# Kernel tuning notes

Hardware: AMD Instinct MI355X
Metric: run time of the kernel (lower is better)

Reference implementation:

```python
import jax, jax.numpy as jnp
import numpy as np
from jax import lax

N = 1_000_000   # nodes
E = 16_000_000  # edges
K1, K2, K3 = 100_000, 10_000, 2_500  # ceil(ratio*n) per pooling stage
EPS = 1e-5


def cgconv(x, src, dst, edge_attr, edge_valid, Wf, bf, Ws, bs, gamma, beta, num_nodes):
    # z_ij = [x_i, x_j, e_ij]  (PyG: i = target = dst, j = source = src)
    z = jnp.concatenate([x[dst], x[src], edge_attr], axis=-1)          # [E,3]
    m = jax.nn.sigmoid(z @ Wf + bf) * jax.nn.softplus(z @ Ws + bs)     # [E,1]
    m = m * edge_valid[:, None].astype(m.dtype)
    aggr = jax.ops.segment_sum(m, dst, num_segments=num_nodes)         # [n,1]
    # BatchNorm1d (training-mode batch stats, biased var), then residual
    mean = aggr.mean(axis=0)
    var = aggr.var(axis=0)
    bn = gamma * (aggr - mean) / jnp.sqrt(var + EPS) + beta
    return bn + x


def topk_pool(x, src, dst, edge_attr, edge_valid, w, k, num_nodes):
    # Original torch code broadcasts x[N,1]*w[C] -> sum(-1) == x*sum(w); tanh nonlinearity.
    score = jnp.tanh(x[:, 0] * jnp.sum(w) / jnp.linalg.norm(w))        # [n]
    top_scores, perm = lax.top_k(score, k)
    x_new = x[perm] * top_scores[:, None]
    mask = jnp.zeros((num_nodes,), bool).at[perm].set(True)
    new_idx = jnp.zeros((num_nodes,), jnp.int32).at[perm].set(jnp.arange(k, dtype=jnp.int32))
    ev = edge_valid & mask[src] & mask[dst]
    return x_new, new_idx[src], new_idx[dst], edge_attr, ev


def setup_inputs() -> dict:
    key = jax.random.key(0)
    ks = jax.random.split(key, 24)
    d = {}
    d["x"] = jax.random.normal(ks[0], (N, 1), jnp.float32)
    d["edge_attr"] = jax.random.uniform(ks[1], (E, 1), jnp.float32)
    d["src"] = jax.random.randint(ks[2], (E,), 0, N, jnp.int32)
    d["dst"] = jax.random.randint(ks[3], (E,), 0, N, jnp.int32)
    d["batch"] = jnp.zeros((N,), jnp.int32)
    p = lambda k, shp: jax.random.normal(k, shp, jnp.float32) * 0.1
    d["Wf1"], d["bf1"] = p(ks[4], (3, 1)), p(ks[5], (1,))
    d["Ws1"], d["bs1"] = p(ks[6], (3, 1)), p(ks[7], (1,))
    d["g1"], d["be1"] = jnp.ones((1,), jnp.float32), jnp.zeros((1,), jnp.float32)
    d["Wf2"], d["bf2"] = p(ks[8], (3, 1)), p(ks[9], (1,))
    d["Ws2"], d["bs2"] = p(ks[10], (3, 1)), p(ks[11], (1,))
    d["g2"], d["be2"] = jnp.ones((1,), jnp.float32), jnp.zeros((1,), jnp.float32)
    d["pw1"] = p(ks[12], (800,))
    d["pw2"] = p(ks[13], (80,))
    d["pw3"] = p(ks[14], (8,))
    d["Wl1"], d["bl1"] = p(ks[15], (1, 8)), p(ks[16], (8,))
    d["Wl2"], d["bl2"] = p(ks[17], (8, 2)), p(ks[18], (2,))
    return d


def reference(x, edge_attr, Wf1, bf1, Ws1, bs1, g1, be1, Wf2, bf2, Ws2, bs2, g2, be2,
              pw1, pw2, pw3, Wl1, bl1, Wl2, bl2, src, dst, batch):
    ev = jnp.ones((E,), bool)
    x = cgconv(x, src, dst, edge_attr, ev, Wf1, bf1, Ws1, bs1, g1, be1, N)
    x, s, dd, ea, ev = topk_pool(x, src, dst, edge_attr, ev, pw1, K1, N)
    x = cgconv(x, s, dd, ea, ev, Wf2, bf2, Ws2, bs2, g2, be2, K1)
    x, s, dd, ea, ev = topk_pool(x, s, dd, ea, ev, pw2, K2, K1)
    x, s, dd, ea, ev = topk_pool(x, s, dd, ea, ev, pw3, K3, K2)
    h = jax.nn.relu(x @ Wl1 + bl1)
    # dropout is identity in eval/reference mode
    return jax.nn.log_softmax(h @ Wl2 + bl2, axis=1)
```

## Files before the change

### kernel.cpp

```cpp
#include <hip/hip_runtime.h>
#include <math.h>

#define CHUNK 4096
#define NB2   256
#define BSH   12
#define CAP   24
#define CAPW  49
#define FG    16
#define RND   1024
#define EPB   16384

typedef int      i32x4 __attribute__((ext_vector_type(4)));
typedef float    f32x4 __attribute__((ext_vector_type(4)));
typedef unsigned u32x2 __attribute__((ext_vector_type(2)));

__device__ __forceinline__ i32x4 ntld4i(const int* p)   { return __builtin_nontemporal_load((const i32x4*)p); }
__device__ __forceinline__ f32x4 ntld4f(const float* p) { return __builtin_nontemporal_load((const f32x4*)p); }

__device__ __forceinline__ float sigmoidf_(float x) {
    if (x >= 0.0f) { float e = expf(-x); return 1.0f / (1.0f + e); }
    float e = expf(x); return e / (1.0f + e);
}
__device__ __forceinline__ float softplusf_(float x) {
    return fmaxf(x, 0.0f) + log1pf(expf(-fabsf(x)));
}
__device__ __forceinline__ unsigned key_desc(float f) {
    unsigned u = __float_as_uint(f);
    unsigned ka = (u & 0x80000000u) ? ~u : (u | 0x80000000u);
    return ~ka;
}
__device__ __forceinline__ float edge_m(float xd, float xs, float a,
                                        float wf0, float wf1, float wf2, float b0,
                                        float ws0, float ws1, float ws2, float b1) {
    float f = xd * wf0 + xs * wf1 + a * wf2 + b0;
    float g = xd * ws0 + xs * ws1 + a * ws2 + b1;
    return sigmoidf_(f) * softplusf_(g);
}

__global__ void k_consts(const float* __restrict__ pw1, const float* __restrict__ pw2,
                         const float* __restrict__ pw3, float* __restrict__ consts,
                         int n1, int n2, int n3) {
    const float* w; int n;
    if (blockIdx.x == 0)      { w = pw1; n = n1; }
    else if (blockIdx.x == 1) { w = pw2; n = n2; }
    else                      { w = pw3; n = n3; }
    __shared__ float s1[256], s2[256];
    float a = 0.f, b = 0.f;
    for (int i = threadIdx.x; i < n; i += 256) { float v = w[i]; a += v; b += v * v; }
    s1[threadIdx.x] = a; s2[threadIdx.x] = b; __syncthreads();
    for (int o = 128; o > 0; o >>= 1) {
        if (threadIdx.x < o) { s1[threadIdx.x] += s1[threadIdx.x + o]; s2[threadIdx.x] += s2[threadIdx.x + o]; }
        __syncthreads();
    }
    if (threadIdx.x == 0) consts[blockIdx.x] = s1[0] / sqrtf(s2[0]);
}

__global__ void __launch_bounds__(256) k_ehist2(const int* __restrict__ dst,
                                                unsigned* __restrict__ hist,
                                                int e0, int e1) {
    __shared__ unsigned h[NB2];
    int t = threadIdx.x;
    h[t] = 0;
    __syncthreads();
    int cs = e0 + blockIdx.x * EPB;
    int ce = cs + EPB; if (ce > e1) ce = e1;
    for (int eb = cs; eb < ce; eb += RND) {
        int i = eb + t * 4;
        if (eb + RND <= ce) {
            i32x4 d4 = ntld4i(dst + i);
            atomicAdd(&h[((unsigned)d4.x) >> BSH], 1u);
            atomicAdd(&h[((unsigned)d4.y) >> BSH], 1u);
            atomicAdd(&h[((unsigned)d4.z) >> BSH], 1u);
            atomicAdd(&h[((unsigned)d4.w) >> BSH], 1u);
        } else {
            #pragma unroll
            for (int j = 0; j < 4; ++j)
                if (i + j < ce) atomicAdd(&h[((unsigned)dst[i + j]) >> BSH], 1u);
        }
    }
    __syncthreads();
    hist[(size_t)blockIdx.x * NB2 + t] = h[t];
}

__global__ void k_scanA(const unsigned* __restrict__ hist, unsigned* __restrict__ offs,
                        unsigned* __restrict__ tot, int G) {
    int d = blockIdx.x, ND = gridDim.x, t = threadIdx.x;
    __shared__ unsigned s[256];
    unsigned carry = 0;
    for (int tile = 0; tile * 256 < G; ++tile) {
        int g = tile * 256 + t;
        unsigned v = (g < G) ? hist[(size_t)g * ND + d] : 0u;
        s[t] = v; __syncthreads();
        for (int o = 1; o < 256; o <<= 1) {
            unsigned u = (t >= o) ? s[t - o] : 0u;
            __syncthreads();
            s[t] += u; __syncthreads();
        }
        if (g < G) offs[(size_t)g * ND + d] = s[t] - v + carry;
        unsigned tl = s[255]; __syncthreads();
        carry += tl;
    }
    if (t == 0) tot[d] = carry;
}

__global__ void k_scanB(const unsigned* __restrict__ tot, unsigned* __restrict__ base,
                        int ND, unsigned rmask) {
    __shared__ unsigned s[256];
    int t = threadIdx.x;
    unsigned carry = 0;
    for (int tile = 0; tile * 256 < ND; ++tile) {
        int d = tile * 256 + t;
        unsigned v = (d < ND) ? ((tot[d] + rmask) & ~rmask) : 0u;
        s[t] = v; __syncthreads();
        for (int o = 1; o < 256; o <<= 1) {
            unsigned u = (t >= o) ? s[t - o] : 0u;
            __syncthreads();
            s[t] += u; __syncthreads();
        }
        if (d < ND) base[d] = s[t] - v + carry;
        unsigned tl = s[255]; __syncthreads();
        carry += tl;
    }
    if (t == 0) base[ND] = carry;
}

__global__ void __launch_bounds__(256) k_part(
        const float* __restrict__ x, const float* __restrict__ ea,
        const int* __restrict__ src, const int* __restrict__ dst,
        const float* __restrict__ Wf, const float* __restrict__ bf,
        const float* __restrict__ Ws, const float* __restrict__ bs,
        const unsigned* __restrict__ offs, const unsigned* __restrict__ binBase,
        uint2* __restrict__ rec, int e0, int e1) {
    __shared__ unsigned stage[NB2 * CAPW];
    __shared__ unsigned gcur[NB2], fil[NB2];
    int t = threadIdx.x;
    gcur[t] = binBase[t] + offs[(size_t)blockIdx.x * NB2 + t];
    fil[t] = 0;
    __syncthreads();
    int cs = e0 + blockIdx.x * EPB;
    int ce = cs + EPB; if (ce > e1) ce = e1;
    float wf0 = Wf[0], wf1 = Wf[1], wf2 = Wf[2], b0 = bf[0];
    float ws0 = Ws[0], ws1 = Ws[1], ws2 = Ws[2], b1 = bs[0];
    for (int rb = cs; rb < ce; rb += RND) {
        int s4[4], d4[4]; float a4[4]; bool vl[4];
        int eb = rb + t * 4;
        if (rb + RND <= ce) {
            i32x4 sv = ntld4i(src + eb);
            i32x4 dv = ntld4i(dst + eb);
            f32x4 av = ntld4f(ea + eb);
            s4[0]=sv.x; s4[1]=sv.y; s4[2]=sv.z; s4[3]=sv.w;
            d4[0]=dv.x; d4[1]=dv.y; d4[2]=dv.z; d4[3]=dv.w;
            a4[0]=av.x; a4[1]=av.y; a4[2]=av.z; a4[3]=av.w;
            vl[0]=vl[1]=vl[2]=vl[3]=true;
        } else {
            #pragma unroll
            for (int j = 0; j < 4; ++j) {
                int e = eb + j;
                vl[j] = e < ce;
                s4[j] = vl[j] ? src[e] : 0;
                d4[j] = vl[j] ? dst[e] : 0;
                a4[j] = vl[j] ? ea[e]  : 0.f;
            }
        }
        #pragma unroll
        for (int j = 0; j < 4; ++j) {
            if (!vl[j]) continue;
            int d = d4[j];
            float m = edge_m(x[d], x[s4[j]], a4[j], wf0, wf1, wf2, b0, ws0, ws1, ws2, b1);
            unsigned bin = ((unsigned)d) >> BSH;
            unsigned dl  = (unsigned)(d & ((1 << BSH) - 1));
            unsigned slot = atomicAdd(&fil[bin], 1u);
            if (slot < CAP) {
                stage[bin * CAPW + 2 * slot]     = __float_as_uint(m);
                stage[bin * CAPW + 2 * slot + 1] = dl;
            } else {
                rec[gcur[bin] + slot] = make_uint2(__float_as_uint(m), dl);
            }
        }
        __syncthreads();
        {
            unsigned c = fil[t], g = gcur[t];
            unsigned* st = &stage[t * CAPW];
            if (c > CAP) {
                for (unsigned k = 0; k < CAP; ++k)
                    rec[g + k] = make_uint2(st[2 * k], st[2 * k + 1]);
                gcur[t] = g + c; fil[t] = 0;
            } else {
                unsigned ngrp = c >> 4;
                if (ngrp) {
                    unsigned nfl = ngrp << 4;
                    for (unsigned k = 0; k < nfl; ++k)
                        rec[g + k] = make_uint2(st[2 * k], st[2 * k + 1]);
                    unsigned rem = c - nfl;
                    for (unsigned k = 0; k < rem; ++k) {
                        st[2 * k]     = st[2 * (nfl + k)];
                        st[2 * k + 1] = st[2 * (nfl + k) + 1];
                    }
                    gcur[t] = g + nfl; fil[t] = rem;
                }
            }
        }
        __syncthreads();
    }
    {
        unsigned c = fil[t], g = gcur[t];
        unsigned* st = &stage[t * CAPW];
        unsigned cc = c < CAP ? c : CAP;
        for (unsigned k = 0; k < cc; ++k)
            rec[g + k] = make_uint2(st[2 * k], st[2 * k + 1]);
    }
}

__global__ void __launch_bounds__(256) k_aggr2(
        const uint2* __restrict__ rec, const unsigned* __restrict__ base,
        const unsigned* __restrict__ tot, float* __restrict__ aggr,
        float* __restrict__ stats, int N, int accumulate, int doStats) {
    __shared__ float acc[1 << BSH];
    int t = threadIdx.x, b = blockIdx.x;
    for (int i = t; i < (1 << BSH); i += 256) acc[i] = 0.f;
    __syncthreads();
    unsigned lo = base[b], hi = lo + tot[b];
    for (unsigned i = lo + t; i < hi; i += 256) {
        u32x2 r = __builtin_nontemporal_load((const u32x2*)&rec[i]);
        atomicAdd(&acc[r.y], __uint_as_float(r.x));
    }
    __syncthreads();
    int nb = b << BSH;
    float s = 0.f, q = 0.f;
    for (int i = t; i < (1 << BSH); i += 256) {
        int node = nb + i;
        if (node < N) {
            float v = acc[i];
            if (accumulate) v += aggr[node];
            aggr[node] = v;
            if (doStats) { s += v; q += v * v; }
        }
    }
    if (doStats) {
        __shared__ float s1[256], s2[256];
        s1[t] = s; s2[t] = q; __syncthreads();
        for (int o = 128; o > 0; o >>= 1) {
            if (t < o) { s1[t] += s1[t + o]; s2[t] += s2[t + o]; }
            __syncthreads();
        }
        if (t == 0) { atomicAdd(&stats[0], s1[0]); atomicAdd(&stats[1], s2[0]); }
    }
}

__global__ void k_conv1(const float* __restrict__ x, const float* __restrict__ ea,
                        const int* __restrict__ src, const int* __restrict__ dst,
                        const float* __restrict__ Wf, const float* __restrict__ bf,
                        const float* __restrict__ Ws, const float* __restrict__ bs,
                        float* __restrict__ aggr, int E) {
    int e = blockIdx.x * blockDim.x + threadIdx.x;
    if (e >= E) return;
    int s = src[e], d = dst[e];
    atomicAdd(&aggr[d], edge_m(x[d], x[s], ea[e], Wf[0], Wf[1], Wf[2], bf[0],
                               Ws[0], Ws[1], Ws[2], bs[0]));
}

__global__ void __launch_bounds__(256) k_conv2(
        const float* __restrict__ x2, const float* __restrict__ ea,
        const int* __restrict__ src, const int* __restrict__ dst,
        const int* __restrict__ nidx,
        const float* __restrict__ Wf, const float* __restrict__ bf,
        const float* __restrict__ Ws, const float* __restrict__ bs,
        float* __restrict__ aggr, int E) {
    int base = (blockIdx.x * 256 + threadIdx.x) * 4;
    if (base >= E) return;
    float wf0 = Wf[0], wf1 = Wf[1], wf2 = Wf[2], b0 = bf[0];
    float ws0 = Ws[0], ws1 = Ws[1], ws2 = Ws[2], b1 = bs[0];
    int d4[4]; int cnt;
    if (base + 4 <= E) {
        i32x4 dv = ntld4i(dst + base);
        d4[0]=dv.x; d4[1]=dv.y; d4[2]=dv.z; d4[3]=dv.w;
        cnt = 4;
    } else {
        cnt = E - base;
        for (int j = 0; j < cnt; ++j) d4[j] = dst[base + j];
    }
    #pragma unroll
    for (int j = 0; j < 4; ++j) {
        if (j >= cnt) break;
        int nd = nidx[d4[j]];
        if (nd < 0) continue;
        int sv = __builtin_nontemporal_load(src + base + j);
        int ns = nidx[sv];
        if (ns < 0) continue;
        float a = __builtin_nontemporal_load(ea + base + j);
        atomicAdd(&aggr[nd], edge_m(x2[nd], x2[ns], a, wf0, wf1, wf2, b0, ws0, ws1, ws2, b1));
    }
}

__global__ void k_stats(const float* __restrict__ a, int n, float* __restrict__ stats) {
    float s = 0.f, q = 0.f;
    int stride = gridDim.x * blockDim.x;
    for (int i = blockIdx.x * blockDim.x + threadIdx.x; i < n; i += stride) {
        float v = a[i]; s += v; q += v * v;
    }
    __shared__ float s1[256], s2[256];
    s1[threadIdx.x] = s; s2[threadIdx.x] = q; __syncthreads();
    for (int o = 128; o > 0; o >>= 1) {
        if (threadIdx.x < o) { s1[threadIdx.x] += s1[threadIdx.x + o]; s2[threadIdx.x] += s2[threadIdx.x + o]; }
        __syncthreads();
    }
    if (threadIdx.x == 0) { atomicAdd(&stats[0], s1[0]); atomicAdd(&stats[1], s2[0]); }
}

__global__ void k_bn(const float* __restrict__ aggr, const float* __restrict__ xin,
                     const float* __restrict__ stats, const float* __restrict__ g,
                     const float* __restrict__ be, float* __restrict__ xout,
                     int n, float invn, const float* __restrict__ consts, int ci,
                     unsigned* __restrict__ keys, unsigned* __restrict__ vals) {
    int i = blockIdx.x * blockDim.x + threadIdx.x;
    if (i >= n) return;
    float mean = stats[0] * invn;
    float var  = stats[1] * invn - mean * mean;
    float inv  = 1.0f / sqrtf(var + 1e-5f);
    float v = g[0] * (aggr[i] - mean) * inv + be[0] + xin[i];
    xout[i] = v;
    if (keys) {
        float s = tanhf(v * consts[ci]);
        keys[i] = key_desc(s);
        vals[i] = (unsigned)i;
    }
}

__global__ void k_hist(const unsigned* __restrict__ keys, unsigned* __restrict__ hist,
                       int n, int shift) {
    __shared__ unsigned h[256];
    int t = threadIdx.x;
    h[t] = 0;
    __syncthreads();
    int base = blockIdx.x * CHUNK;
    if (base + CHUNK <= n) {
        #pragma unroll
        for (int it = 0; it < CHUNK / 1024; ++it) {
            int i = base + it * 1024 + t * 4;
            const unsigned* p = keys + i;
            unsigned k0 = p[0], k1 = p[1], k2 = p[2], k3 = p[3];
            atomicAdd(&h[(k0 >> shift) & 255u], 1u);
            atomicAdd(&h[(k1 >> shift) & 255u], 1u);
            atomicAdd(&h[(k2 >> shift) & 255u], 1u);
            atomicAdd(&h[(k3 >> shift) & 255u], 1u);
        }
    } else {
        int end = n;
        for (int i = base + t; i < end; i += 256)
            atomicAdd(&h[(keys[i] >> shift) & 255u], 1u);
    }
    __syncthreads();
    hist[blockIdx.x * 256 + t] = h[t];
}

__global__ void __launch_bounds__(256) k_scatter(const unsigned* __restrict__ keys,
                                                 const unsigned* __restrict__ vals,
                                                 unsigned* __restrict__ okeys,
                                                 unsigned* __restrict__ ovals,
                                                 const unsigned* __restrict__ offs,
                                                 const unsigned* __restrict__ base_,
                                                 int n, int shift) {
    __shared__ unsigned run[256];
    __shared__ unsigned offl[256];
    __shared__ unsigned wcnt[4][256];
    __shared__ unsigned wpre[4][256];
    int t = threadIdx.x;
    int wave = t >> 6, lane = t & 63;
    run[t] = 0;
    offl[t] = offs[(size_t)blockIdx.x * 256 + t] + base_[t];
    __syncthreads();
    int cbase = blockIdx.x * CHUNK;
    const int GROUPS = CHUNK / 256;
    for (int gix = 0; gix < GROUPS; ++gix) {
        int i = cbase + gix * 256 + t;
        bool active = i < n;
        unsigned k = active ? keys[i] : 0u;
        unsigned v = active ? vals[i] : 0u;
        unsigned d = (k >> shift) & 255u;
        unsigned long long amask = __ballot(active);
        unsigned long long bb[8];
        #pragma unroll
        for (int bit = 0; bit < 8; ++bit) bb[bit] = __ballot(active && ((d >> bit) & 1u));
        unsigned long long m = amask;
        #pragma unroll
        for (int bit = 0; bit < 8; ++bit) m &= ((d >> bit) & 1u) ? bb[bit] : ~bb[bit];
        unsigned rk = (unsigned)__popcll(m & ((1ull << lane) - 1ull));
        #pragma unroll
        for (int j = 0; j < 4; ++j) {
            unsigned dd = (unsigned)lane + j * 64u;
            unsigned long long mm = amask;
            #pragma unroll
            for (int bit = 0; bit < 8; ++bit) mm &= ((dd >> bit) & 1u) ? bb[bit] : ~bb[bit];
            wcnt[wave][dd] = (unsigned)__popcll(mm);
        }
        __syncthreads();
        {
            unsigned r = run[t];
            unsigned c0 = wcnt[0][t], c1 = wcnt[1][t], c2 = wcnt[2][t], c3 = wcnt[3][t];
            wpre[0][t] = r;
            wpre[1][t] = r + c0;
            wpre[2][t] = r + c0 + c1;
            wpre[3][t] = r + c0 + c1 + c2;
            run[t] = r + c0 + c1 + c2 + c3;
        }
        __syncthreads();
        if (active) {
            unsigned pos = offl[d] + wpre[wave][d] + rk;
            okeys[pos] = k;
            ovals[pos] = v;
        }
    }
}

__global__ void k_pool(const unsigned* __restrict__ perm, const float* __restrict__ xin,
                       const float* __restrict__ consts, int ci,
                       float* __restrict__ xout, int* __restrict__ newidx, int k,
                       unsigned* __restrict__ okeys, unsigned* __restrict__ ovals, int nci) {
    int r = blockIdx.x * blockDim.x + threadIdx.x;
    if (r >= k) return;
    unsigned p = perm[r];
    float xv = xin[p];
    float s = tanhf(xv * consts[ci]);
    float o = xv * s;
    xout[r] = o;
    if (newidx) newidx[p] = r;
    if (okeys) {
        float s2 = tanhf(o * consts[nci]);
        okeys[r] = key_desc(s2);
        ovals[r] = (unsigned)r;
    }
}

__global__ void __launch_bounds__(1024) k_smallsort(
        unsigned* __restrict__ kIn, unsigned* __restrict__ vIn,
        unsigned* __restrict__ kTmp, unsigned* __restrict__ vTmp,
        int n, int k3, const float* __restrict__ xin,
        const float* __restrict__ consts, int ci,
        const float* __restrict__ Wl1, const float* __restrict__ bl1,
        const float* __restrict__ Wl2, const float* __restrict__ bl2,
        float* __restrict__ out) {
    __shared__ unsigned hist[256], sc[256], run[256], offl[256];
    __shared__ unsigned wcnt[16][256];
    __shared__ unsigned wpre[16][256];
    int t = threadIdx.x;
    int wave = t >> 6, lane = t & 63;
    unsigned *ki = kIn, *vi = vIn, *ko = kTmp, *vo = vTmp;
    for (int p = 0; p < 4; ++p) {
        int shift = p * 8;
        if (t < 256) hist[t] = 0;
        __syncthreads();
        for (int i = t; i < n; i += 1024)
            atomicAdd(&hist[(ki[i] >> shift) & 255u], 1u);
        __syncthreads();
        if (t < 256) sc[t] = hist[t];
        __syncthreads();
        for (int o = 1; o < 256; o <<= 1) {
            unsigned u = 0;
            if (t < 256 && t >= o) u = sc[t - o];
            __syncthreads();
            if (t < 256) sc[t] += u;
            __syncthreads();
        }
        if (t < 256) { offl[t] = sc[t] - hist[t]; run[t] = 0; }
        __syncthreads();
        int G = (n + 1023) / 1024;
        for (int gix = 0; gix < G; ++gix) {
            int i = gix * 1024 + t;
            bool active = i < n;
            unsigned k = active ? ki[i] : 0u;
            unsigned v = active ? vi[i] : 0u;
            unsigned d = (k >> shift) & 255u;
            unsigned long long amask = __ballot(active);
            unsigned long long bb[8];
            #pragma unroll
            for (int bit = 0; bit < 8; ++bit) bb[bit] = __ballot(active && ((d >> bit) & 1u));
            unsigned long long m = amask;
            #pragma unroll
            for (int bit = 0; bit < 8; ++bit) m &= ((d >> bit) & 1u) ? bb[bit] : ~bb[bit];
            unsigned rk = (unsigned)__popcll(m & ((1ull << lane) - 1ull));
            #pragma unroll
            for (int j = 0; j < 4; ++j) {
                unsigned dd = (unsigned)lane + j * 64u;
                unsigned long long mm = amask;
                #pragma unroll
                for (int bit = 0; bit < 8; ++bit) mm &= ((dd >> bit) & 1u) ? bb[bit] : ~bb[bit];
                wcnt[wave][dd] = (unsigned)__popcll(mm);
            }
            __syncthreads();
            if (t < 256) {
                unsigned acc = run[t];
                #pragma unroll
                for (int w2 = 0; w2 < 16; ++w2) { wpre[w2][t] = acc; acc += wcnt[w2][t]; }
                run[t] = acc;
            }
            __syncthreads();
            if (active) {
                unsigned pos = offl[d] + wpre[wave][d] + rk;
                ko[pos] = k;
                vo[pos] = v;
            }
            __syncthreads();
        }
        unsigned* tp;
        tp = ki; ki = ko; ko = tp;
        tp = vi; vi = vo; vo = tp;
        __syncthreads();
    }
    float c = consts[ci];
    float b20 = bl2[0], b21 = bl2[1];
    for (int r = t; r < k3; r += 1024) {
        unsigned pidx = vIn[r];
        float xv = xin[pidx];
        float s = tanhf(xv * c);
        float o = xv * s;
        float l0 = b20, l1 = b21;
        #pragma unroll
        for (int j = 0; j < 8; ++j) {
            float h = fmaxf(o * Wl1[j] + bl1[j], 0.0f);
            l0 += h * Wl2[2 * j];
            l1 += h * Wl2[2 * j + 1];
        }
        float mx = fmaxf(l0, l1);
        float lse = mx + logf(expf(l0 - mx) + expf(l1 - mx));
        out[2 * r]     = l0 - lse;
        out[2 * r + 1] = l1 - lse;
    }
}

static void sort_pairs(hipStream_t stream, unsigned* kA, unsigned* vA,
                       unsigned* kB, unsigned* vB, unsigned* hist, unsigned* offs,
                       unsigned* tot, unsigned* base, int n) {
    int G = (n + CHUNK - 1) / CHUNK;
    unsigned *ki = kA, *vi = vA, *ko = kB, *vo = vB;
    for (int p = 0; p < 4; ++p) {
        int shift = p * 8;
        k_hist<<<G, 256, 0, stream>>>(ki, hist, n, shift);
        k_scanA<<<256, 256, 0, stream>>>(hist, offs, tot, G);
        k_scanB<<<1, 256, 0, stream>>>(tot, base, 256, 0u);
        k_scatter<<<G, 256, 0, stream>>>(ki, vi, ko, vo, offs, base, n, shift);
        unsigned* t;
        t = ki; ki = ko; ko = t;
        t = vi; vi = vo; vo = t;
    }
}

extern "C" void kernel_launch(void* const* d_in, const int* in_sizes, int n_in,
                              void* d_out, int out_size, void* d_ws, size_t ws_size,
                              hipStream_t stream) {
    const float* x   = (const float*)d_in[0];
    const float* ea  = (const float*)d_in[1];
    const int*   src = (const int*)d_in[2];
    const int*   dst = (const int*)d_in[3];
    const float *Wf1 = (const float*)d_in[5],  *bf1 = (const float*)d_in[6];
    const float *Ws1 = (const float*)d_in[7],  *bs1 = (const float*)d_in[8];
    const float *g1  = (const float*)d_in[9],  *be1 = (const float*)d_in[10];
    const float *Wf2 = (const float*)d_in[11], *bf2 = (const float*)d_in[12];
    const float *Ws2 = (const float*)d_in[13], *bs2 = (const float*)d_in[14];
    const float *g2  = (const float*)d_in[15], *be2 = (const float*)d_in[16];
    const float *pw1 = (const float*)d_in[17], *pw2 = (const float*)d_in[18], *pw3 = (const float*)d_in[19];
    const float *Wl1 = (const float*)d_in[20], *bl1 = (const float*)d_in[21];
    const float *Wl2 = (const float*)d_in[22], *bl2 = (const float*)d_in[23];

    const int N  = in_sizes[0];
    const int E  = in_sizes[1];
    const int K1 = 100000, K2 = 10000, K3 = 2500;

    size_t off = 0;
    auto alloc = [&](size_t bytes) { size_t o = off; off = (off + bytes + 255) & ~(size_t)255; return o; };
    char* ws = (char*)d_ws;
    size_t o_x1    = alloc((size_t)N * 4);
    size_t o_nidx  = alloc((size_t)N * 4);
    size_t o_stats = alloc(256);
    size_t o_const = alloc(256);
    size_t o_tot   = alloc(4096);
    size_t o_base  = alloc(8192);
    size_t o_x2    = alloc((size_t)K1 * 4);
    size_t o_x3    = alloc((size_t)K1 * 4);
    size_t o_ag2   = alloc((size_t)K1 * 4);
    size_t o_x4    = alloc((size_t)K2 * 4);
    size_t o_x5    = alloc((size_t)K3 * 4);
    size_t o_ag1   = alloc((size_t)N * 4);
    size_t o_arena = off;

    int G1 = (N + CHUNK - 1) / CHUNK;
    size_t s_kA = 0;
    size_t s_vA = s_kA + (((size_t)N * 4 + 255) & ~(size_t)255);
    size_t s_kB = s_vA + (((size_t)N * 4 + 255) & ~(size_t)255);
    size_t s_vB = s_kB + (((size_t)N * 4 + 255) & ~(size_t)255);
    size_t s_h  = s_vB + (((size_t)N * 4 + 255) & ~(size_t)255);
    size_t s_o  = s_h  + (((size_t)G1 * 256 * 4 + 255) & ~(size_t)255);
    size_t sortSz = s_o + (size_t)G1 * 256 * 4;

    int H = 0, Eh = 0;
    size_t p_rec = 0, p_eh = 0, p_eo = 0;
    for (int h = 1; h <= 8; h <<= 1) {
        int eh_ = (E + h - 1) / h;
        eh_ = (eh_ + RND - 1) & ~(RND - 1);
        int gc_ = (eh_ + EPB - 1) / EPB;
        size_t recB = (((size_t)(eh_ + NB2 * FG) * 8) + 255) & ~(size_t)255;
        size_t ehB  = (((size_t)gc_ * NB2 * 4) + 255) & ~(size_t)255;
        size_t eoB  = (((size_t)gc_ * NB2 * 4) + 255) & ~(size_t)255;
        size_t partSz = recB + ehB + eoB;
        size_t arenaSz = partSz > sortSz ? partSz : sortSz;
        if (o_arena + arenaSz <= ws_size && N <= (NB2 << BSH)) {
            H = h; Eh = eh_;
            p_rec = 0; p_eh = p_rec + recB; p_eo = p_eh + ehB;
            break;
        }
    }

    float*    x1     = (float*)(ws + o_x1);
    int*      nidx   = (int*)(ws + o_nidx);
    float*    stats  = (float*)(ws + o_stats);
    float*    consts = (float*)(ws + o_const);
    unsigned* tot    = (unsigned*)(ws + o_tot);
    unsigned* base   = (unsigned*)(ws + o_base);
    float*    x2     = (float*)(ws + o_x2);
    float*    x3     = (float*)(ws + o_x3);
    float*    aggr2  = (float*)(ws + o_ag2);
    float*    x4     = (float*)(ws + o_x4);
    float*    aggr1  = (float*)(ws + o_ag1);
    unsigned* kA     = (unsigned*)(ws + o_arena + s_kA);
    unsigned* vA     = (unsigned*)(ws + o_arena + s_vA);
    unsigned* kB     = (unsigned*)(ws + o_arena + s_kB);
    unsigned* vB     = (unsigned*)(ws + o_arena + s_vB);
    unsigned* hist   = (unsigned*)(ws + o_arena + s_h);
    unsigned* offs   = (unsigned*)(ws + o_arena + s_o);

    hipMemsetAsync(nidx, 0xFF, (size_t)N * 4, stream);
    hipMemsetAsync(stats, 0, 64, stream);
    hipMemsetAsync(aggr2, 0, (size_t)K1 * 4, stream);

    k_consts<<<3, 256, 0, stream>>>(pw1, pw2, pw3, consts,
                                    in_sizes[17], in_sizes[18], in_sizes[19]);

    if (H > 0) {
        uint2*    rec = (uint2*)(ws + o_arena + p_rec);
        unsigned* eh  = (unsigned*)(ws + o_arena + p_eh);
        unsigned* eo  = (unsigned*)(ws + o_arena + p_eo);
        int NBN = (N + (1 << BSH) - 1) >> BSH;
        for (int h = 0; h < H; ++h) {
            int e0 = h * Eh;
            int e1 = e0 + Eh; if (e1 > E) e1 = E;
            if (e0 >= e1) break;
            int GCh = (e1 - e0 + EPB - 1) / EPB;
            k_ehist2<<<GCh, 256, 0, stream>>>(dst, eh, e0, e1);
            k_scanA<<<NB2, 256, 0, stream>>>(eh, eo, tot, GCh);
            k_scanB<<<1, 256, 0, stream>>>(tot, base, NB2, (unsigned)(FG - 1));
            k_part<<<GCh, 256, 0, stream>>>(x, ea, src, dst, Wf1, bf1, Ws1, bs1,
                                            eo, base, rec, e0, e1);
            k_aggr2<<<NBN, 256, 0, stream>>>(rec, base, tot, aggr1, stats, N,
                                             h > 0, h == H - 1 ? 1 : 0);
        }
    } else {
        hipMemsetAsync(aggr1, 0, (size_t)N * 4, stream);
        k_conv1<<<(E + 255) / 256, 256, 0, stream>>>(x, ea, src, dst, Wf1, bf1, Ws1, bs1, aggr1, E);
        k_stats<<<1024, 256, 0, stream>>>(aggr1, N, stats);
    }
    k_bn<<<(N + 255) / 256, 256, 0, stream>>>(aggr1, x, stats, g1, be1, x1, N, 1.0f / (float)N,
                                              consts, 0, kA, vA);

    sort_pairs(stream, kA, vA, kB, vB, hist, offs, tot, base, N);
    k_pool<<<(K1 + 255) / 256, 256, 0, stream>>>(vA, x1, consts, 0, x2, nidx, K1,
                                                 (unsigned*)nullptr, (unsigned*)nullptr, 0);

    k_conv2<<<(E / 4 + 255) / 256, 256, 0, stream>>>(x2, ea, src, dst, nidx,
                                                     Wf2, bf2, Ws2, bs2, aggr2, E);
    k_stats<<<256, 256, 0, stream>>>(aggr2, K1, stats + 2);
    k_bn<<<(K1 + 255) / 256, 256, 0, stream>>>(aggr2, x2, stats + 2, g2, be2, x3, K1, 1.0f / (float)K1,
                                               consts, 1, kA, vA);

    sort_pairs(stream, kA, vA, kB, vB, hist, offs, tot, base, K1);
    k_pool<<<(K2 + 255) / 256, 256, 0, stream>>>(vA, x3, consts, 1, x4, (int*)nullptr, K2,
                                                 kB, vB, 2);

    k_smallsort<<<1, 1024, 0, stream>>>(kB, vB, kA, vA, K2, K3, x4, consts, 2,
                                        Wl1, bl1, Wl2, bl2, (float*)d_out);
}
```

Baseline: 902.3 us.

## Fold bin-base scans into consumers, drop memsets, and cooperatively flush stage buffers

Removes the single-block k_scanB launches. Each consumer block (k_part, k_aggr2, k_scatter) now recomputes the 256-entry exclusive scan of totals in shared memory. The three memsets are folded into k_consts and k_bn initialization, which cuts the kernel launch count. The k_part staging flush now uses 16-lane groups per bin instead of one serial thread per bin, and k_conv2 loads src with vector loads. The trade-off is redundant per-block scans and an extra barrier sequence in each block.

```diff
diff --git a/kernel.cpp b/kernel.cpp
--- a/kernel.cpp
+++ b/kernel.cpp
@@ -39,7 +39,8 @@
 
 __global__ void k_consts(const float* __restrict__ pw1, const float* __restrict__ pw2,
                          const float* __restrict__ pw3, float* __restrict__ consts,
-                         int n1, int n2, int n3) {
+                         float* __restrict__ stats, int n1, int n2, int n3) {
+    if (blockIdx.x == 0 && threadIdx.x < 16) stats[threadIdx.x] = 0.f;
     const float* w; int n;
     if (blockIdx.x == 0)      { w = pw1; n = n1; }
     else if (blockIdx.x == 1) { w = pw2; n = n2; }
@@ -103,44 +104,33 @@
     if (t == 0) tot[d] = carry;
 }
 
-__global__ void k_scanB(const unsigned* __restrict__ tot, unsigned* __restrict__ base,
-                        int ND, unsigned rmask) {
-    __shared__ unsigned s[256];
-    int t = threadIdx.x;
-    unsigned carry = 0;
-    for (int tile = 0; tile * 256 < ND; ++tile) {
-        int d = tile * 256 + t;
-        unsigned v = (d < ND) ? ((tot[d] + rmask) & ~rmask) : 0u;
-        s[t] = v; __syncthreads();
-        for (int o = 1; o < 256; o <<= 1) {
-            unsigned u = (t >= o) ? s[t - o] : 0u;
-            __syncthreads();
-            s[t] += u; __syncthreads();
-        }
-        if (d < ND) base[d] = s[t] - v + carry;
-        unsigned tl = s[255]; __syncthreads();
-        carry += tl;
-    }
-    if (t == 0) base[ND] = carry;
-}
-
 __global__ void __launch_bounds__(256) k_part(
         const float* __restrict__ x, const float* __restrict__ ea,
         const int* __restrict__ src, const int* __restrict__ dst,
         const float* __restrict__ Wf, const float* __restrict__ bf,
         const float* __restrict__ Ws, const float* __restrict__ bs,
-        const unsigned* __restrict__ offs, const unsigned* __restrict__ binBase,
+        const unsigned* __restrict__ offs, const unsigned* __restrict__ tot,
         uint2* __restrict__ rec, int e0, int e1) {
     __shared__ unsigned stage[NB2 * CAPW];
     __shared__ unsigned gcur[NB2], fil[NB2];
     int t = threadIdx.x;
-    gcur[t] = binBase[t] + offs[(size_t)blockIdx.x * NB2 + t];
-    fil[t] = 0;
+    {
+        unsigned v = (tot[t] + FG - 1) & ~(unsigned)(FG - 1);
+        stage[t] = v; __syncthreads();
+        for (int o = 1; o < 256; o <<= 1) {
+            unsigned u = (t >= o) ? stage[t - o] : 0u;
+            __syncthreads();
+            stage[t] += u; __syncthreads();
+        }
+        gcur[t] = (stage[t] - v) + offs[(size_t)blockIdx.x * NB2 + t];
+        fil[t] = 0;
+    }
     __syncthreads();
     int cs = e0 + blockIdx.x * EPB;
     int ce = cs + EPB; if (ce > e1) ce = e1;
     float wf0 = Wf[0], wf1 = Wf[1], wf2 = Wf[2], b0 = bf[0];
     float ws0 = Ws[0], ws1 = Ws[1], ws2 = Ws[2], b1 = bs[0];
+    int sg = t >> 4, ln = t & 15;
     for (int rb = cs; rb < ce; rb += RND) {
         int s4[4], d4[4]; float a4[4]; bool vl[4];
         int eb = rb + t * 4;
@@ -178,48 +168,57 @@
             }
         }
         __syncthreads();
-        {
-            unsigned c = fil[t], g = gcur[t];
-            unsigned* st = &stage[t * CAPW];
+        for (int i = 0; i < NB2 / 16; ++i) {
+            int b = sg + (i << 4);
+            unsigned c = fil[b];
+            if (c < FG) continue;
+            unsigned g = gcur[b];
+            unsigned* st = &stage[b * CAPW];
             if (c > CAP) {
-                for (unsigned k = 0; k < CAP; ++k)
-                    rec[g + k] = make_uint2(st[2 * k], st[2 * k + 1]);
-                gcur[t] = g + c; fil[t] = 0;
+                rec[g + ln] = make_uint2(st[2 * ln], st[2 * ln + 1]);
+                if (ln < CAP - 16)
+                    rec[g + 16 + ln] = make_uint2(st[2 * (16 + ln)], st[2 * (16 + ln) + 1]);
+                if (ln == 0) { gcur[b] = g + c; fil[b] = 0; }
             } else {
-                unsigned ngrp = c >> 4;
-                if (ngrp) {
-                    unsigned nfl = ngrp << 4;
-                    for (unsigned k = 0; k < nfl; ++k)
-                        rec[g + k] = make_uint2(st[2 * k], st[2 * k + 1]);
-                    unsigned rem = c - nfl;
-                    for (unsigned k = 0; k < rem; ++k) {
-                        st[2 * k]     = st[2 * (nfl + k)];
-                        st[2 * k + 1] = st[2 * (nfl + k) + 1];
-                    }
-                    gcur[t] = g + nfl; fil[t] = rem;
-                }
+                rec[g + ln] = make_uint2(st[2 * ln], st[2 * ln + 1]);
+                unsigned rem = c - FG;
+                unsigned lo0 = 0, lo1 = 0;
+                if (ln < rem) { lo0 = st[2 * (FG + ln)]; lo1 = st[2 * (FG + ln) + 1]; }
+                if (ln < rem) { st[2 * ln] = lo0; st[2 * ln + 1] = lo1; }
+                if (ln == 0) { gcur[b] = g + FG; fil[b] = rem; }
             }
         }
         __syncthreads();
     }
+    for (int i = 0; i < NB2 / 16; ++i) {
+        int b = sg + (i << 4);
+        unsigned c = fil[b], g = gcur[b];
+        unsigned* st = &stage[b * CAPW];
+        if (ln < c) rec[g + ln] = make_uint2(st[2 * ln], st[2 * ln + 1]);
+    }
+}
+
+__global__ void __launch_bounds__(256) k_aggr2(
+        const uint2* __restrict__ rec, const unsigned* __restrict__ tot,
+        float* __restrict__ aggr, float* __restrict__ stats,
+        int N, int accumulate, int doStats) {
+    __shared__ float acc[1 << BSH];
+    __shared__ unsigned sc[256];
+    __shared__ unsigned sBase, sCnt;
+    int t = threadIdx.x, b = blockIdx.x;
     {
-        unsigned c = fil[t], g = gcur[t];
-        unsigned* st = &stage[t * CAPW];
-        unsigned cc = c < CAP ? c : CAP;
-        for (unsigned k = 0; k < cc; ++k)
-            rec[g + k] = make_uint2(st[2 * k], st[2 * k + 1]);
-    }
-}
-
-__global__ void __launch_bounds__(256) k_aggr2(
-        const uint2* __restrict__ rec, const unsigned* __restrict__ base,
-        const unsigned* __restrict__ tot, float* __restrict__ aggr,
-        float* __restrict__ stats, int N, int accumulate, int doStats) {
-    __shared__ float acc[1 << BSH];
-    int t = threadIdx.x, b = blockIdx.x;
+        unsigned v = (tot[t] + FG - 1) & ~(unsigned)(FG - 1);
+        sc[t] = v; __syncthreads();
+        for (int o = 1; o < 256; o <<= 1) {
+            unsigned u = (t >= o) ? sc[t - o] : 0u;
+            __syncthreads();
+            sc[t] += u; __syncthreads();
+        }
+        if (t == b) { sBase = sc[t] - v; sCnt = tot[t]; }
+    }
     for (int i = t; i < (1 << BSH); i += 256) acc[i] = 0.f;
     __syncthreads();
-    unsigned lo = base[b], hi = lo + tot[b];
+    unsigned lo = sBase, hi = lo + sCnt;
     for (unsigned i = lo + t; i < hi; i += 256) {
         u32x2 r = __builtin_nontemporal_load((const u32x2*)&rec[i]);
         atomicAdd(&acc[r.y], __uint_as_float(r.x));
@@ -270,22 +269,23 @@
     if (base >= E) return;
     float wf0 = Wf[0], wf1 = Wf[1], wf2 = Wf[2], b0 = bf[0];
     float ws0 = Ws[0], ws1 = Ws[1], ws2 = Ws[2], b1 = bs[0];
-    int d4[4]; int cnt;
+    int d4[4], s4[4]; int cnt;
     if (base + 4 <= E) {
         i32x4 dv = ntld4i(dst + base);
+        i32x4 sv = ntld4i(src + base);
         d4[0]=dv.x; d4[1]=dv.y; d4[2]=dv.z; d4[3]=dv.w;
+        s4[0]=sv.x; s4[1]=sv.y; s4[2]=sv.z; s4[3]=sv.w;
         cnt = 4;
     } else {
         cnt = E - base;
-        for (int j = 0; j < cnt; ++j) d4[j] = dst[base + j];
+        for (int j = 0; j < cnt; ++j) { d4[j] = dst[base + j]; s4[j] = src[base + j]; }
     }
     #pragma unroll
     for (int j = 0; j < 4; ++j) {
         if (j >= cnt) break;
         int nd = nidx[d4[j]];
         if (nd < 0) continue;
-        int sv = __builtin_nontemporal_load(src + base + j);
-        int ns = nidx[sv];
+        int ns = nidx[s4[j]];
         if (ns < 0) continue;
         float a = __builtin_nontemporal_load(ea + base + j);
         atomicAdd(&aggr[nd], edge_m(x2[nd], x2[ns], a, wf0, wf1, wf2, b0, ws0, ws1, ws2, b1));
@@ -311,19 +311,20 @@
                      const float* __restrict__ stats, const float* __restrict__ g,
                      const float* __restrict__ be, float* __restrict__ xout,
                      int n, float invn, const float* __restrict__ consts, int ci,
-                     unsigned* __restrict__ keys, unsigned* __restrict__ vals) {
+                     unsigned* __restrict__ keys, unsigned* __restrict__ vals,
+                     int* __restrict__ nidxInit, float* __restrict__ zeroArr, int nZero) {
     int i = blockIdx.x * blockDim.x + threadIdx.x;
     if (i >= n) return;
+    if (nidxInit) nidxInit[i] = -1;
+    if (zeroArr && i < nZero) zeroArr[i] = 0.f;
     float mean = stats[0] * invn;
     float var  = stats[1] * invn - mean * mean;
     float inv  = 1.0f / sqrtf(var + 1e-5f);
     float v = g[0] * (aggr[i] - mean) * inv + be[0] + xin[i];
     xout[i] = v;
-    if (keys) {
-        float s = tanhf(v * consts[ci]);
-        keys[i] = key_desc(s);
-        vals[i] = (unsigned)i;
-    }
+    float s = tanhf(v * consts[ci]);
+    keys[i] = key_desc(s);
+    vals[i] = (unsigned)i;
 }
 
 __global__ void k_hist(const unsigned* __restrict__ keys, unsigned* __restrict__ hist,
@@ -345,8 +346,7 @@
             atomicAdd(&h[(k3 >> shift) & 255u], 1u);
         }
     } else {
-        int end = n;
-        for (int i = base + t; i < end; i += 256)
+        for (int i = base + t; i < n; i += 256)
             atomicAdd(&h[(keys[i] >> shift) & 255u], 1u);
     }
     __syncthreads();
@@ -358,16 +358,26 @@
                                                  unsigned* __restrict__ okeys,
                                                  unsigned* __restrict__ ovals,
                                                  const unsigned* __restrict__ offs,
-                                                 const unsigned* __restrict__ base_,
+                                                 const unsigned* __restrict__ tot,
                                                  int n, int shift) {
     __shared__ unsigned run[256];
     __shared__ unsigned offl[256];
     __shared__ unsigned wcnt[4][256];
     __shared__ unsigned wpre[4][256];
+    __shared__ unsigned sc[256];
     int t = threadIdx.x;
     int wave = t >> 6, lane = t & 63;
-    run[t] = 0;
-    offl[t] = offs[(size_t)blockIdx.x * 256 + t] + base_[t];
+    {
+        unsigned v = tot[t];
+        sc[t] = v; __syncthreads();
+        for (int o = 1; o < 256; o <<= 1) {
+            unsigned u = (t >= o) ? sc[t - o] : 0u;
+            __syncthreads();
+            sc[t] += u; __syncthreads();
+        }
+        offl[t] = offs[(size_t)blockIdx.x * 256 + t] + (sc[t] - v);
+        run[t] = 0;
+    }
     __syncthreads();
     int cbase = blockIdx.x * CHUNK;
     const int GROUPS = CHUNK / 256;
@@ -529,15 +539,14 @@
 
 static void sort_pairs(hipStream_t stream, unsigned* kA, unsigned* vA,
                        unsigned* kB, unsigned* vB, unsigned* hist, unsigned* offs,
-                       unsigned* tot, unsigned* base, int n) {
+                       unsigned* tot, int n) {
     int G = (n + CHUNK - 1) / CHUNK;
     unsigned *ki = kA, *vi = vA, *ko = kB, *vo = vB;
     for (int p = 0; p < 4; ++p) {
         int shift = p * 8;
         k_hist<<<G, 256, 0, stream>>>(ki, hist, n, shift);
         k_scanA<<<256, 256, 0, stream>>>(hist, offs, tot, G);
-        k_scanB<<<1, 256, 0, stream>>>(tot, base, 256, 0u);
-        k_scatter<<<G, 256, 0, stream>>>(ki, vi, ko, vo, offs, base, n, shift);
+        k_scatter<<<G, 256, 0, stream>>>(ki, vi, ko, vo, offs, tot, n, shift);
         unsigned* t;
         t = ki; ki = ko; ko = t;
         t = vi; vi = vo; vo = t;
@@ -573,12 +582,10 @@
     size_t o_stats = alloc(256);
     size_t o_const = alloc(256);
     size_t o_tot   = alloc(4096);
-    size_t o_base  = alloc(8192);
     size_t o_x2    = alloc((size_t)K1 * 4);
     size_t o_x3    = alloc((size_t)K1 * 4);
     size_t o_ag2   = alloc((size_t)K1 * 4);
     size_t o_x4    = alloc((size_t)K2 * 4);
-    size_t o_x5    = alloc((size_t)K3 * 4);
     size_t o_ag1   = alloc((size_t)N * 4);
     size_t o_arena = off;
 
@@ -614,7 +621,6 @@
     float*    stats  = (float*)(ws + o_stats);
     float*    consts = (float*)(ws + o_const);
     unsigned* tot    = (unsigned*)(ws + o_tot);
-    unsigned* base   = (unsigned*)(ws + o_base);
     float*    x2     = (float*)(ws + o_x2);
     float*    x3     = (float*)(ws + o_x3);
     float*    aggr2  = (float*)(ws + o_ag2);
@@ -627,11 +633,7 @@
     unsigned* hist   = (unsigned*)(ws + o_arena + s_h);
     unsigned* offs   = (unsigned*)(ws + o_arena + s_o);
 
-    hipMemsetAsync(nidx, 0xFF, (size_t)N * 4, stream);
-    hipMemsetAsync(stats, 0, 64, stream);
-    hipMemsetAsync(aggr2, 0, (size_t)K1 * 4, stream);
-
-    k_consts<<<3, 256, 0, stream>>>(pw1, pw2, pw3, consts,
+    k_consts<<<3, 256, 0, stream>>>(pw1, pw2, pw3, consts, stats,
                                     in_sizes[17], in_sizes[18], in_sizes[19]);
 
     if (H > 0) {
@@ -646,10 +648,9 @@
             int GCh = (e1 - e0 + EPB - 1) / EPB;
             k_ehist2<<<GCh, 256, 0, stream>>>(dst, eh, e0, e1);
             k_scanA<<<NB2, 256, 0, stream>>>(eh, eo, tot, GCh);
-            k_scanB<<<1, 256, 0, stream>>>(tot, base, NB2, (unsigned)(FG - 1));
             k_part<<<GCh, 256, 0, stream>>>(x, ea, src, dst, Wf1, bf1, Ws1, bs1,
-                                            eo, base, rec, e0, e1);
-            k_aggr2<<<NBN, 256, 0, stream>>>(rec, base, tot, aggr1, stats, N,
+                                            eo, tot, rec, e0, e1);
+            k_aggr2<<<NBN, 256, 0, stream>>>(rec, tot, aggr1, stats, N,
                                              h > 0, h == H - 1 ? 1 : 0);
         }
     } else {
@@ -658,9 +659,9 @@
         k_stats<<<1024, 256, 0, stream>>>(aggr1, N, stats);
     }
     k_bn<<<(N + 255) / 256, 256, 0, stream>>>(aggr1, x, stats, g1, be1, x1, N, 1.0f / (float)N,
-                                              consts, 0, kA, vA);
-
-    sort_pairs(stream, kA, vA, kB, vB, hist, offs, tot, base, N);
+                                              consts, 0, kA, vA, nidx, aggr2, K1);
+
+    sort_pairs(stream, kA, vA, kB, vB, hist, offs, tot, N);
     k_pool<<<(K1 + 255) / 256, 256, 0, stream>>>(vA, x1, consts, 0, x2, nidx, K1,
                                                  (unsigned*)nullptr, (unsigned*)nullptr, 0);
 
@@ -668,9 +669,10 @@
                                                      Wf2, bf2, Ws2, bs2, aggr2, E);
     k_stats<<<256, 256, 0, stream>>>(aggr2, K1, stats + 2);
     k_bn<<<(K1 + 255) / 256, 256, 0, stream>>>(aggr2, x2, stats + 2, g2, be2, x3, K1, 1.0f / (float)K1,
-                                               consts, 1, kA, vA);
-
-    sort_pairs(stream, kA, vA, kB, vB, hist, offs, tot, base, K1);
+                                               consts, 1, kA, vA,
+                                               (int*)nullptr, (float*)nullptr, 0);
+
+    sort_pairs(stream, kA, vA, kB, vB, hist, offs, tot, K1);
     k_pool<<<(K2 + 255) / 256, 256, 0, stream>>>(vA, x3, consts, 1, x4, (int*)nullptr, K2,
                                                  kB, vB, 2);
 
```

Measured after the change: 882.7 us. 2.2% less time.
